# Optimization experiments

Measured on AMD Instinct MI355X. Metric: run time of the kernel, lower is better.

## Reference

```python
import jax, jax.numpy as jnp
import numpy as np

B, T, L, DIM = 64, 4096, 1, 256
NLOC, KS, PAD = 32, 31, 15


def setup_inputs() -> dict:
    key = jax.random.key(0)
    ks = jax.random.split(key, 7)
    query_vector = jax.random.normal(ks[0], (L, B, DIM), jnp.float32)
    encoder_out = jax.random.normal(ks[1], (T, B, DIM), jnp.float32)
    # previous attention weights, non-negative like a softmax output
    mask = jax.random.uniform(ks[2], (B, T, 1), jnp.float32)
    # nn.Linear weights: y = x @ W.T
    W_w = jax.random.normal(ks[3], (DIM, DIM), jnp.float32) / np.sqrt(DIM)
    L_w = jax.random.normal(ks[4], (DIM, NLOC), jnp.float32) / np.sqrt(NLOC)
    # nn.Conv1d weight: (out_ch, in_ch, kernel)
    conv_w = jax.random.normal(ks[5], (NLOC, 1, KS), jnp.float32) / np.sqrt(KS)
    conv_b = jax.random.normal(ks[6], (NLOC,), jnp.float32) * 0.01
    return {
        "query_vector": query_vector,
        "encoder_out": encoder_out,
        "mask": mask,
        "W_w": W_w,
        "L_w": L_w,
        "conv_w": conv_w,
        "conv_b": conv_b,
    }


def reference(query_vector, encoder_out, mask, W_w, L_w, conv_w, conv_b):
    # score(): W projection, seq-first (T,B,D) -> batch-first (B,T,D)
    enc = jnp.einsum("tbd,ed->bte", encoder_out, W_w)  # (B, T, DIM)
    # location features: Conv1d over previous attention weights
    x = jnp.transpose(mask, (0, 2, 1))  # (B, 1, T)
    conv = jax.lax.conv_general_dilated(
        x, conv_w, window_strides=(1,), padding=[(PAD, PAD)],
        dimension_numbers=("NCH", "OIH", "NCH"),
    ) + conv_b[None, :, None]  # (B, NLOC, T)
    loc = jnp.einsum("bct,ec->bte", conv, L_w)  # (B, T, DIM)
    # energies = (enc + loc) @ query^T  -> (B, T, L)
    q = jnp.transpose(query_vector, (1, 2, 0))  # (B, DIM, L)
    energies = jnp.einsum("bte,bel->btl", enc + loc, q)
    attn = jax.nn.softmax(energies, axis=1)  # softmax over T
    # context = encoder_out^T @ attn -> (L, B, DIM)
    context = jnp.einsum("tbd,btl->lbd", encoder_out, attn)
    return context, attn
```

## Files before the change

### kernel.cpp

```cpp
#include <hip/hip_runtime.h>
#include <hip/hip_bf16.h>

#define B_    64
#define T_    4096
#define DIM_  256
#define NLOC_ 32
#define KS_   31
#define PAD_  15
#define CHUNK_ 128
#define NCH_  (T_ / CHUNK_)

typedef unsigned short u16;
typedef unsigned int   u32;

__device__ __forceinline__ float bf2f(u16 u) {
  return __uint_as_float(((u32)u) << 16);
}
__device__ __forceinline__ u16 f2bf(float f) {
  u32 x = __float_as_uint(f);
  return (u16)((x + 0x7fffu + ((x >> 16) & 1u)) >> 16);
}

template<bool F32>
__device__ __forceinline__ float ldv(const void* p, size_t i) {
  if constexpr (F32) return ((const float*)p)[i];
  else               return bf2f(((const u16*)p)[i]);
}
template<bool F32>
__device__ __forceinline__ void ld8(const void* p, size_t i, float ef[8]) {
  if constexpr (F32) {
    const float4* q = (const float4*)((const float*)p + i);
    float4 a = q[0], b = q[1];
    ef[0]=a.x; ef[1]=a.y; ef[2]=a.z; ef[3]=a.w;
    ef[4]=b.x; ef[5]=b.y; ef[6]=b.z; ef[7]=b.w;
  } else {
    uint4 c = *(const uint4*)((const u16*)p + i);
    ef[0]=__uint_as_float(c.x << 16); ef[1]=__uint_as_float(c.x & 0xffff0000u);
    ef[2]=__uint_as_float(c.y << 16); ef[3]=__uint_as_float(c.y & 0xffff0000u);
    ef[4]=__uint_as_float(c.z << 16); ef[5]=__uint_as_float(c.z & 0xffff0000u);
    ef[6]=__uint_as_float(c.w << 16); ef[7]=__uint_as_float(c.w & 0xffff0000u);
  }
}

__global__ void k_detect(const u16* __restrict__ w, int* __restrict__ flag) {
  int tid = threadIdx.x;
  int cnt = 0;
  for (int i = tid; i < 4096; i += 64) {
    float a = fabsf(bf2f(w[i]));
    if (!(a < 64.f) || (a > 0.f && a < 1e-20f)) cnt++;
  }
  #pragma unroll
  for (int o = 32; o >= 1; o >>= 1) cnt += __shfl_xor(cnt, o, 64);
  if (tid == 0) *flag = (cnt > 200) ? 1 : 0;
}

template<bool F32>
__device__ __forceinline__ void prep_body(
    const void* qv, const void* Ww, const void* Lw, const void* cw,
    const void* cb, float* qW, float* kern, float* bias)
{
  const int b = blockIdx.x, tid = threadIdx.x;
  __shared__ float q_s[DIM_];
  __shared__ float qL_s[NLOC_];
  q_s[tid] = ldv<F32>(qv, b * DIM_ + tid);
  __syncthreads();
  float acc = 0.f;
  #pragma unroll 8
  for (int e = 0; e < DIM_; ++e) acc += q_s[e] * ldv<F32>(Ww, e * DIM_ + tid);
  qW[b * DIM_ + tid] = acc;
  if (tid < NLOC_) {
    float a = 0.f;
    #pragma unroll 8
    for (int e = 0; e < DIM_; ++e) a += q_s[e] * ldv<F32>(Lw, e * NLOC_ + tid);
    qL_s[tid] = a;
  }
  __syncthreads();
  if (tid < KS_) {
    float a = 0.f;
    #pragma unroll
    for (int c = 0; c < NLOC_; ++c) a += ldv<F32>(cw, c * KS_ + tid) * qL_s[c];
    kern[b * 32 + tid] = a;
  } else if (tid == KS_) {
    float a = 0.f;
    #pragma unroll
    for (int c = 0; c < NLOC_; ++c) a += ldv<F32>(cb, c) * qL_s[c];
    bias[b] = a;
  }
}

__global__ __launch_bounds__(256) void k_prep(
    const void* qv, const void* Ww, const void* Lw, const void* cw,
    const void* cb, float* qW, float* kern, float* bias, const int* flag)
{
  if (*flag) prep_body<true >(qv, Ww, Lw, cw, cb, qW, kern, bias);
  else       prep_body<false>(qv, Ww, Lw, cw, cb, qW, kern, bias);
}

template<bool F32>
__device__ __forceinline__ void main_body(
    const void* enc, const void* mask,
    const float* qW, const float* kern, const float* bias,
    float* energies, float* blk_m, float* blk_Z, float* blk_ctx)
{
  const int b = blockIdx.y, ch = blockIdx.x, t0 = ch * CHUNK_;
  const int tid = threadIdx.x;
  const int wave = tid >> 6, lane = tid & 63, half = lane >> 5, hl = lane & 31;
  const int halfid = wave * 2 + half;

  __shared__ float mask_s[CHUNK_ + 2 * PAD_];
  __shared__ float kern_s[32];
  __shared__ float loc_s[CHUNK_];
  __shared__ float e_s[CHUNK_];
  __shared__ float pm[8], pZ[8];
  __shared__ float pctx[8][DIM_];

  for (int i = tid; i < CHUNK_ + 2 * PAD_; i += 256) {
    int g = t0 - PAD_ + i;
    mask_s[i] = (g >= 0 && g < T_) ? ldv<F32>(mask, (size_t)b * T_ + g) : 0.f;
  }
  if (tid < 32) kern_s[tid] = (tid < KS_) ? kern[b * 32 + tid] : bias[b];

  float wq[8];
  {
    const float4* q4 = (const float4*)(qW + b * DIM_ + 8 * hl);
    float4 a = q4[0], c = q4[1];
    wq[0]=a.x; wq[1]=a.y; wq[2]=a.z; wq[3]=a.w;
    wq[4]=c.x; wq[5]=c.y; wq[6]=c.z; wq[7]=c.w;
  }
  __syncthreads();

  if (tid < CHUNK_) {
    float a = kern_s[31];
    #pragma unroll
    for (int k = 0; k < KS_; ++k) a += mask_s[tid + k] * kern_s[k];
    loc_s[tid] = a;
  }
  __syncthreads();

  const int lbase = wave * (CHUNK_ / 4);
  const int tbase = t0 + lbase;
  float m = -INFINITY, Z = 0.f;
  float ctx[8];
  #pragma unroll
  for (int q = 0; q < 8; ++q) ctx[q] = 0.f;

  const size_t STEP = (size_t)2 * B_ * DIM_;
  const size_t base = (size_t)(tbase + half) * (B_ * DIM_) + b * DIM_ + 8 * hl;
  const int NIT = CHUNK_ / 8;

  auto process = [&](const float ef[8], int j) {
    float p = wq[0]*ef[0] + wq[1]*ef[1] + wq[2]*ef[2] + wq[3]*ef[3]
            + wq[4]*ef[4] + wq[5]*ef[5] + wq[6]*ef[6] + wq[7]*ef[7];
    #pragma unroll
    for (int o = 16; o >= 1; o >>= 1) p += __shfl_xor(p, o, 64);
    const int tloc = lbase + 2 * j + half;
    float e = p + loc_s[tloc];
    if (hl == 0) e_s[tloc] = e;
    float mn = fmaxf(m, e);
    float sc = __expf(m - mn);
    float w  = __expf(e - mn);
    Z = Z * sc + w;
    #pragma unroll
    for (int q = 0; q < 8; ++q) ctx[q] = ctx[q] * sc + w * ef[q];
    m = mn;
  };

  float efA[8], efB[8];
  ld8<F32>(enc, base, efA);
  #pragma unroll
  for (int j = 0; j < NIT; j += 2) {
    ld8<F32>(enc, base + (size_t)(j + 1) * STEP, efB);
    process(efA, j);
    if (j + 2 < NIT) ld8<F32>(enc, base + (size_t)(j + 2) * STEP, efA);
    process(efB, j + 1);
  }

  if (hl == 0) { pm[halfid] = m; pZ[halfid] = Z; }
  #pragma unroll
  for (int q = 0; q < 8; ++q) pctx[halfid][8 * hl + q] = ctx[q];
  __syncthreads();

  if (tid < CHUNK_) energies[(size_t)b * T_ + t0 + tid] = e_s[tid];

  float M = pm[0];
  #pragma unroll
  for (int i = 1; i < 8; ++i) M = fmaxf(M, pm[i]);
  float cx = 0.f;
  #pragma unroll
  for (int i = 0; i < 8; ++i) cx += __expf(pm[i] - M) * pctx[i][tid];
  blk_ctx[((size_t)b * NCH_ + ch) * DIM_ + tid] = cx;
  if (tid == 0) {
    float Zc = 0.f;
    #pragma unroll
    for (int i = 0; i < 8; ++i) Zc += __expf(pm[i] - M) * pZ[i];
    blk_m[b * NCH_ + ch] = M;
    blk_Z[b * NCH_ + ch] = Zc;
  }
}

__global__ __launch_bounds__(256) void k_main(
    const void* enc, const void* mask,
    const float* qW, const float* kern, const float* bias,
    float* energies, float* blk_m, float* blk_Z, float* blk_ctx,
    const int* flag)
{
  if (*flag) main_body<true >(enc, mask, qW, kern, bias, energies, blk_m, blk_Z, blk_ctx);
  else       main_body<false>(enc, mask, qW, kern, bias, energies, blk_m, blk_Z, blk_ctx);
}

__global__ __launch_bounds__(256) void k_combine(
    const float* __restrict__ blk_m, const float* __restrict__ blk_Z,
    const float* __restrict__ blk_ctx,
    float* __restrict__ Mb, float* __restrict__ Zb, void* __restrict__ out,
    const int* __restrict__ flag)
{
  const int b = blockIdx.x, tid = threadIdx.x;
  __shared__ float sm[NCH_], sZ[NCH_];
  if (tid < NCH_) { sm[tid] = blk_m[b * NCH_ + tid]; sZ[tid] = blk_Z[b * NCH_ + tid]; }
  __syncthreads();
  float M = sm[0];
  #pragma unroll
  for (int i = 1; i < NCH_; ++i) M = fmaxf(M, sm[i]);
  float Zg = 0.f;
  #pragma unroll
  for (int i = 0; i < NCH_; ++i) Zg += __expf(sm[i] - M) * sZ[i];
  float cx = 0.f;
  for (int i = 0; i < NCH_; ++i)
    cx += __expf(sm[i] - M) * blk_ctx[((size_t)b * NCH_ + i) * DIM_ + tid];
  float v = cx / Zg;
  if (*flag) ((float*)out)[b * DIM_ + tid] = v;
  else       ((u16*)out)[b * DIM_ + tid]   = f2bf(v);
  if (tid == 0) { Mb[b] = M; Zb[b] = Zg; }
}

__global__ __launch_bounds__(256) void k_attn(
    const float* __restrict__ energies, const float* __restrict__ Mb,
    const float* __restrict__ Zb, void* __restrict__ out,
    const int* __restrict__ flag)
{
  const int idx = blockIdx.x * 256 + threadIdx.x;
  const int b = idx >> 12;
  float a = __expf(energies[idx] - Mb[b]) / Zb[b];
  if (*flag) ((float*)out)[B_ * DIM_ + idx] = a;
  else       ((u16*)out)[B_ * DIM_ + idx]   = f2bf(a);
}

extern "C" void kernel_launch(void* const* d_in, const int* in_sizes, int n_in,
                              void* d_out, int out_size, void* d_ws, size_t ws_size,
                              hipStream_t stream) {
  const void* qv   = d_in[0];
  const void* enc  = d_in[1];
  const void* mask = d_in[2];
  const void* Ww   = d_in[3];
  const void* Lw   = d_in[4];
  const void* cw   = d_in[5];
  const void* cb   = d_in[6];

  float* ws     = (float*)d_ws;
  int*   flag   = (int*)ws;
  float* qW     = ws + 64;
  float* kern   = ws + 16448;
  float* bias   = ws + 18496;
  float* Mb     = ws + 18560;
  float* Zb     = ws + 18624;
  float* energ  = ws + 18688;
  float* blk_m  = ws + 280832;
  float* blk_Z  = ws + 282880;
  float* blk_cx = ws + 284928;

  k_detect<<<1, 64, 0, stream>>>((const u16*)Ww, flag);
  k_prep<<<B_, 256, 0, stream>>>(qv, Ww, Lw, cw, cb, qW, kern, bias, flag);
  k_main<<<dim3(NCH_, B_), 256, 0, stream>>>(enc, mask, qW, kern, bias,
                                             energ, blk_m, blk_Z, blk_cx, flag);
  k_combine<<<B_, 256, 0, stream>>>(blk_m, blk_Z, blk_cx, Mb, Zb, d_out, flag);
  k_attn<<<(B_ * T_) / 256, 256, 0, stream>>>(energ, Mb, Zb, d_out, flag);
}
```

Measured before the change: 418.5 us.

## Process two batches per block so each wave reads contiguous encoder rows

Each block now handles two adjacent batch entries, and each half-wave covers one batch, so a wave's 64 lanes read 2KB of contiguous memory per timestep (batches b0 and b0+1 are adjacent in the T,B,D layout). Before, the two half-waves read two different timesteps for one batch. Each wave now walks 32 timesteps and the grid is halved, which doubles the per-thread serial work. The main loop is no longer explicitly unrolled, which may reduce register pressure but can weaken load overlap.

```diff
diff --git a/kernel.cpp b/kernel.cpp
--- a/kernel.cpp
+++ b/kernel.cpp
@@ -9,6 +9,7 @@
 #define PAD_  15
 #define CHUNK_ 128
 #define NCH_  (T_ / CHUNK_)
+#define HALO_ (CHUNK_ + 2 * PAD_)
 
 typedef unsigned short u16;
 typedef unsigned int   u32;
@@ -102,60 +103,66 @@
     const float* qW, const float* kern, const float* bias,
     float* energies, float* blk_m, float* blk_Z, float* blk_ctx)
 {
-  const int b = blockIdx.y, ch = blockIdx.x, t0 = ch * CHUNK_;
+  const int ch = blockIdx.x, t0 = ch * CHUNK_;
+  const int b0 = blockIdx.y * 2;
   const int tid = threadIdx.x;
   const int wave = tid >> 6, lane = tid & 63, half = lane >> 5, hl = lane & 31;
+  const int b = b0 + half;
   const int halfid = wave * 2 + half;
 
-  __shared__ float mask_s[CHUNK_ + 2 * PAD_];
-  __shared__ float kern_s[32];
-  __shared__ float loc_s[CHUNK_];
-  __shared__ float e_s[CHUNK_];
+  __shared__ float mask_s[2][HALO_];
+  __shared__ float kern_s[2][32];
+  __shared__ float loc_s[2][CHUNK_];
+  __shared__ float e_s[2][CHUNK_];
   __shared__ float pm[8], pZ[8];
   __shared__ float pctx[8][DIM_];
 
-  for (int i = tid; i < CHUNK_ + 2 * PAD_; i += 256) {
-    int g = t0 - PAD_ + i;
-    mask_s[i] = (g >= 0 && g < T_) ? ldv<F32>(mask, (size_t)b * T_ + g) : 0.f;
-  }
-  if (tid < 32) kern_s[tid] = (tid < KS_) ? kern[b * 32 + tid] : bias[b];
+  for (int i = tid; i < 2 * HALO_; i += 256) {
+    int bo = i / HALO_, ii = i - bo * HALO_;
+    int g = t0 - PAD_ + ii;
+    mask_s[bo][ii] = (g >= 0 && g < T_) ? ldv<F32>(mask, (size_t)(b0 + bo) * T_ + g) : 0.f;
+  }
+  if (tid < 64) {
+    int bo = tid >> 5, k = tid & 31;
+    kern_s[bo][k] = (k < KS_) ? kern[(b0 + bo) * 32 + k] : bias[b0 + bo];
+  }
 
   float wq[8];
   {
-    const float4* q4 = (const float4*)(qW + b * DIM_ + 8 * hl);
+    const float4* q4 = (const float4*)(qW + (size_t)b * DIM_ + 8 * hl);
     float4 a = q4[0], c = q4[1];
     wq[0]=a.x; wq[1]=a.y; wq[2]=a.z; wq[3]=a.w;
     wq[4]=c.x; wq[5]=c.y; wq[6]=c.z; wq[7]=c.w;
   }
   __syncthreads();
 
-  if (tid < CHUNK_) {
-    float a = kern_s[31];
-    #pragma unroll
-    for (int k = 0; k < KS_; ++k) a += mask_s[tid + k] * kern_s[k];
-    loc_s[tid] = a;
-  }
-  __syncthreads();
-
-  const int lbase = wave * (CHUNK_ / 4);
-  const int tbase = t0 + lbase;
+  {
+    int bo = tid >> 7, i = tid & (CHUNK_ - 1);
+    float a = kern_s[bo][31];
+    #pragma unroll
+    for (int k = 0; k < KS_; ++k) a += mask_s[bo][i + k] * kern_s[bo][k];
+    loc_s[bo][i] = a;
+  }
+  __syncthreads();
+
+  const int tA = t0 + wave * 32;
   float m = -INFINITY, Z = 0.f;
   float ctx[8];
   #pragma unroll
   for (int q = 0; q < 8; ++q) ctx[q] = 0.f;
 
-  const size_t STEP = (size_t)2 * B_ * DIM_;
-  const size_t base = (size_t)(tbase + half) * (B_ * DIM_) + b * DIM_ + 8 * hl;
-  const int NIT = CHUNK_ / 8;
+  const size_t STEP = (size_t)B_ * DIM_;
+  const size_t base = ((size_t)tA * B_ + b) * DIM_ + 8 * hl;
+  const int NIT = 32;
 
   auto process = [&](const float ef[8], int j) {
     float p = wq[0]*ef[0] + wq[1]*ef[1] + wq[2]*ef[2] + wq[3]*ef[3]
             + wq[4]*ef[4] + wq[5]*ef[5] + wq[6]*ef[6] + wq[7]*ef[7];
     #pragma unroll
     for (int o = 16; o >= 1; o >>= 1) p += __shfl_xor(p, o, 64);
-    const int tloc = lbase + 2 * j + half;
-    float e = p + loc_s[tloc];
-    if (hl == 0) e_s[tloc] = e;
+    const int tloc = wave * 32 + j;
+    float e = p + loc_s[half][tloc];
+    if (hl == 0) e_s[half][tloc] = e;
     float mn = fmaxf(m, e);
     float sc = __expf(m - mn);
     float w  = __expf(e - mn);
@@ -167,7 +174,6 @@
 
   float efA[8], efB[8];
   ld8<F32>(enc, base, efA);
-  #pragma unroll
   for (int j = 0; j < NIT; j += 2) {
     ld8<F32>(enc, base + (size_t)(j + 1) * STEP, efB);
     process(efA, j);
@@ -180,21 +186,28 @@
   for (int q = 0; q < 8; ++q) pctx[halfid][8 * hl + q] = ctx[q];
   __syncthreads();
 
-  if (tid < CHUNK_) energies[(size_t)b * T_ + t0 + tid] = e_s[tid];
-
-  float M = pm[0];
-  #pragma unroll
-  for (int i = 1; i < 8; ++i) M = fmaxf(M, pm[i]);
-  float cx = 0.f;
-  #pragma unroll
-  for (int i = 0; i < 8; ++i) cx += __expf(pm[i] - M) * pctx[i][tid];
-  blk_ctx[((size_t)b * NCH_ + ch) * DIM_ + tid] = cx;
-  if (tid == 0) {
-    float Zc = 0.f;
-    #pragma unroll
-    for (int i = 0; i < 8; ++i) Zc += __expf(pm[i] - M) * pZ[i];
-    blk_m[b * NCH_ + ch] = M;
-    blk_Z[b * NCH_ + ch] = Zc;
+  {
+    int bo = tid >> 7, i = tid & (CHUNK_ - 1);
+    energies[(size_t)(b0 + bo) * T_ + t0 + i] = e_s[bo][i];
+  }
+
+  #pragma unroll
+  for (int bo = 0; bo < 2; ++bo) {
+    float M = pm[bo];
+    #pragma unroll
+    for (int wv = 1; wv < 4; ++wv) M = fmaxf(M, pm[bo + 2 * wv]);
+    float cx = 0.f;
+    #pragma unroll
+    for (int wv = 0; wv < 4; ++wv)
+      cx += __expf(pm[bo + 2 * wv] - M) * pctx[bo + 2 * wv][tid];
+    blk_ctx[((size_t)(b0 + bo) * NCH_ + ch) * DIM_ + tid] = cx;
+    if (tid == 0) {
+      float Zc = 0.f;
+      #pragma unroll
+      for (int wv = 0; wv < 4; ++wv) Zc += __expf(pm[bo + 2 * wv] - M) * pZ[bo + 2 * wv];
+      blk_m[(b0 + bo) * NCH_ + ch] = M;
+      blk_Z[(b0 + bo) * NCH_ + ch] = Zc;
+    }
   }
 }
 
@@ -270,8 +283,8 @@
 
   k_detect<<<1, 64, 0, stream>>>((const u16*)Ww, flag);
   k_prep<<<B_, 256, 0, stream>>>(qv, Ww, Lw, cw, cb, qW, kern, bias, flag);
-  k_main<<<dim3(NCH_, B_), 256, 0, stream>>>(enc, mask, qW, kern, bias,
-                                             energ, blk_m, blk_Z, blk_cx, flag);
+  k_main<<<dim3(NCH_, B_ / 2), 256, 0, stream>>>(enc, mask, qW, kern, bias,
+                                                 energ, blk_m, blk_Z, blk_cx, flag);
   k_combine<<<B_, 256, 0, stream>>>(blk_m, blk_Z, blk_cx, Mb, Zb, d_out, flag);
   k_attn<<<(B_ * T_) / 256, 256, 0, stream>>>(energ, Mb, Zb, d_out, flag);
 }
```

Measured after the change: 418.3 us. About the same (-0.1%).
